# Performance work log

Measured on AMD Instinct MI355X. Metric: run time of the kernel, lower is better.

Reference implementation:

```python
import jax, jax.numpy as jnp
import numpy as np

B, N = 32, 512
NFEAT, NHID, NCLASS, NHEADS = 128, 64, 128, 8
WORK_D, SUB_D = 32, 32
H1, H2, OUT_D = 256, 256, 512
ALPHA = 0.2
NEG = -9e15


def setup_inputs() -> dict:
    key = jax.random.key(0)
    ks = jax.random.split(key, 16)
    return {
        "graph_inf": jax.random.normal(ks[0], (B, N, NFEAT), jnp.float32),
        "graph_matrix": jax.random.randint(ks[1], (B, N, N), 0, 2, jnp.int32),
        "masks": jnp.ones((B, N), jnp.float32),
        "node_order": jax.random.randint(ks[2], (B,), 0, N, jnp.int64),
        "work": jax.random.normal(ks[3], (B, WORK_D), jnp.float32),
        "subtask": jax.random.normal(ks[4], (B, SUB_D), jnp.float32),
        # GAT head params
        "W_heads": jax.random.normal(ks[5], (NHEADS, NFEAT, NHID), jnp.float32) * 0.1,
        "a_heads": jax.random.normal(ks[6], (NHEADS, 2 * NHID), jnp.float32) * 0.1,
        "W_out": jax.random.normal(ks[7], (NHID * NHEADS, NCLASS), jnp.float32) * 0.05,
        "a_out": jax.random.normal(ks[8], (2 * NCLASS,), jnp.float32) * 0.1,
        # MLP encoder params
        "fc1_w": jax.random.normal(ks[9], (NCLASS + WORK_D + SUB_D, H1), jnp.float32) * 0.07,
        "fc1_b": jnp.zeros((H1,), jnp.float32),
        "fc2_w": jax.random.normal(ks[10], (H1, H2), jnp.float32) * 0.06,
        "fc2_b": jnp.zeros((H2,), jnp.float32),
        "fc3_w": jax.random.normal(ks[11], (H2, OUT_D), jnp.float32) * 0.06,
        "fc3_b": jnp.zeros((OUT_D,), jnp.float32),
    }


def _gat_layer(Wh, a1, a2, adj, masks):
    # Wh: [B,N,F]; additive GAT score e_ij = leakyrelu(a1.Wh_i + a2.Wh_j)
    s1 = Wh @ a1  # [B,N]
    s2 = Wh @ a2  # [B,N]
    e = jax.nn.leaky_relu(s1[:, :, None] + s2[:, None, :], ALPHA)  # [B,N,N]
    att = jax.nn.softmax(jnp.where(adj > 0, e, NEG), axis=2)
    h_prime = jnp.einsum('bnm,bmf->bnf', att, Wh)
    return h_prime * masks[:, :, None]


def reference(graph_inf, graph_matrix, masks, node_order, work, subtask,
              W_heads, a_heads, W_out, a_out,
              fc1_w, fc1_b, fc2_w, fc2_b, fc3_w, fc3_b):
    adj = graph_matrix
    # multi-head GAT layer (concat=True -> ELU)
    def head(Wk, ak):
        Wh = jnp.einsum('bnf,fo->bno', graph_inf, Wk)
        return jax.nn.elu(_gat_layer(Wh, ak[:NHID], ak[NHID:], adj, masks))
    xh = jax.vmap(head)(W_heads, a_heads)  # [H,B,N,NHID]
    x = jnp.transpose(xh, (1, 2, 0, 3)).reshape(B, N, NHEADS * NHID)
    # output GAT layer (concat=False)
    Wh = jnp.einsum('bnf,fo->bno', x, W_out)
    x = _gat_layer(Wh, a_out[:NCLASS], a_out[NCLASS:], adj, masks)
    x = x * masks[:, :, None]
    # select subtask node per batch element
    selected = x[jnp.arange(B), node_order]  # [B,NCLASS]
    inf = jnp.concatenate([selected, work, subtask], axis=1)
    h = jax.nn.relu(inf @ fc1_w + fc1_b)
    h = jax.nn.relu(h @ fc2_w + fc2_b)
    out = h @ fc3_w + fc3_b
    return jax.nn.softmax(out, axis=-1)
```

## Files before the change

### kernel.cpp

```cpp
#include <hip/hip_runtime.h>

typedef unsigned short u16;
typedef unsigned int u32;
typedef unsigned long long u64;

typedef __bf16 bf16x8 __attribute__((ext_vector_type(8)));
typedef float f32x4 __attribute__((ext_vector_type(4)));

#define LOG2E 1.44269504088896340736f

__device__ __forceinline__ float b2f(u16 u) {
    u32 x = ((u32)u) << 16;
    return __builtin_bit_cast(float, x);
}
__device__ __forceinline__ u16 f2b(float f) {
    u32 u = __builtin_bit_cast(u32, f);
    u32 r = (u + 0x7fffu + ((u >> 16) & 1u)) >> 16;
    return (u16)r;
}
__device__ __forceinline__ float ld(const void* p, int i, bool bf) {
    return bf ? b2f(((const u16*)p)[i]) : ((const float*)p)[i];
}
__device__ __forceinline__ bool detect_bf16(const void* masks) {
    return ((const u16*)masks)[0] != 0;
}
__device__ __forceinline__ f32x4 mfma16(bf16x8 a, bf16x8 b, f32x4 c) {
    return __builtin_amdgcn_mfma_f32_16x16x32_bf16(a, b, c, 0, 0, 0);
}

__device__ __attribute__((aligned(256))) u32  g_adjm[16384 * 16];
__device__ __attribute__((aligned(256))) u16  g_BT1[512 * 128];
__device__ __attribute__((aligned(256))) u16  g_BT2[128 * 512];
__device__ __attribute__((aligned(256))) u16  g_Xc[32 * 512 * 128];
__device__ __attribute__((aligned(256))) u16  g_xb[16384 * 512];
__device__ __attribute__((aligned(256))) u16  g_Wh2[16384 * 128];
__device__ __attribute__((aligned(256))) float g_s1b[16384];
__device__ __attribute__((aligned(256))) float g_s2b[16384];
__device__ __attribute__((aligned(256))) u16  g_fc1T[256 * 192];
__device__ __attribute__((aligned(256))) u16  g_fc2T[256 * 256];
__device__ __attribute__((aligned(256))) u16  g_fc3T[512 * 256];
__device__ __attribute__((aligned(256))) u16  g_Ahi[32 * 192];
__device__ __attribute__((aligned(256))) u16  g_Alo[32 * 192];
__device__ __attribute__((aligned(256))) u16  g_H1hi[32 * 256];
__device__ __attribute__((aligned(256))) u16  g_H1lo[32 * 256];
__device__ __attribute__((aligned(256))) u16  g_H2hi[32 * 256];
__device__ __attribute__((aligned(256))) u16  g_H2lo[32 * 256];
__device__ __attribute__((aligned(256))) float g_logits[32 * 512];

__global__ __launch_bounds__(256) void prep_kernel(
    const int* __restrict__ adj, const void* __restrict__ Whd,
    const void* __restrict__ Wo, const void* __restrict__ Xin,
    const void* __restrict__ fc1w, const void* __restrict__ fc2w,
    const void* __restrict__ fc3w, const void* __restrict__ masks)
{
    const bool bf = detect_bf16(masks);
    const int blk = blockIdx.x;
    const int tid = threadIdx.x;
    if (blk < 1024) {
        int id = blk * 256 + tid;
        int row = id >> 4, w = id & 15;
        const int4* p = (const int4*)(adj + row * 512 + w * 32);
        int4 v[8];
        #pragma unroll
        for (int s = 0; s < 8; ++s) v[s] = p[s];
        u32 word = 0;
        #pragma unroll
        for (int s = 0; s < 8; ++s) {
            u32 nib = (v[s].x > 0 ? 1u : 0u) | (v[s].y > 0 ? 2u : 0u) |
                      (v[s].z > 0 ? 4u : 0u) | (v[s].w > 0 ? 8u : 0u);
            word |= nib << (4 * s);
        }
        g_adjm[id] = word;
    } else if (blk < 1028) {
        int base = (blk - 1024) * 16384;
        for (int e = base + tid; e < base + 16384; e += 256) {
            int n = e >> 7, k = e & 127;
            g_BT1[e] = f2b(ld(Whd, (n >> 6) * 8192 + k * 64 + (n & 63), bf));
        }
    } else if (blk < 1032) {
        int base = (blk - 1028) * 16384;
        for (int e = base + tid; e < base + 16384; e += 256) {
            int n = e >> 9, k = e & 511;
            g_BT2[e] = f2b(ld(Wo, k * 128 + n, bf));
        }
    } else if (blk < 1288) {
        if (!bf) {
            int base = (blk - 1032) * 8192;
            for (int e = base + tid; e < base + 8192; e += 256)
                g_Xc[e] = f2b(((const float*)Xin)[e]);
        }
    } else if (blk < 1294) {
        int base = (blk - 1288) * 8192;
        for (int e = base + tid; e < base + 8192; e += 256) {
            int n = e / 192, k = e - n * 192;
            g_fc1T[e] = f2b(ld(fc1w, k * 256 + n, bf));
        }
    } else if (blk < 1302) {
        int base = (blk - 1294) * 8192;
        for (int e = base + tid; e < base + 8192; e += 256) {
            int n = e >> 8, k = e & 255;
            g_fc2T[e] = f2b(ld(fc2w, k * 256 + n, bf));
        }
    } else {
        int base = (blk - 1302) * 8192;
        for (int e = base + tid; e < base + 8192; e += 256) {
            int n = e >> 8, k = e & 255;
            g_fc3T[e] = f2b(ld(fc3w, k * 512 + n, bf));
        }
    }
}

__global__ __launch_bounds__(1024, 1) void gat1_kernel(
    const void* __restrict__ Xin, const void* __restrict__ a_heads,
    const void* __restrict__ masks)
{
    __shared__ __attribute__((aligned(16))) u16 WhL[64 * 520];
    __shared__ __attribute__((aligned(16))) u16 As[64 * 136];
    __shared__ __attribute__((aligned(16))) u16 XcL[128 * 136];
    __shared__ float s1p[4][512];
    __shared__ float s2p[4][512];
    __shared__ float E2s[512];
    __shared__ float E2ps[512];

    const bool bf = detect_bf16(masks);
    const int tid = threadIdx.x;
    const int w = tid >> 6, lane = tid & 63;
    const int c = lane & 15, q = lane >> 4;
    const int b = blockIdx.x & 31;
    const int h = blockIdx.x >> 5;

    const u16* Bsrc = bf ? (const u16*)Xin : g_Xc;

    {
        int r = tid >> 4, seg = (tid & 15) * 8;
        *(uint4*)&As[r * 136 + seg] = *(const uint4*)(g_BT1 + (h * 64 + r) * 128 + seg);
    }

    const int wm = w & 3, wn = w >> 2;
    float a1v[4], a2v[4];
    #pragma unroll
    for (int i = 0; i < 4; ++i) {
        int o = wm * 16 + q * 4 + i;
        a1v[i] = ld(a_heads, h * 128 + o, bf);
        a2v[i] = ld(a_heads, h * 128 + 64 + o, bf);
    }

    const int pr = tid >> 3, pseg = (tid & 7) * 16;
    uint4 xr0, xr1;
    {
        const u16* src = Bsrc + (b * 512 + pr) * 128 + pseg;
        xr0 = *(const uint4*)src;
        xr1 = *(const uint4*)(src + 8);
    }

    for (int chunk = 0; chunk < 4; ++chunk) {
        __syncthreads();
        *(uint4*)&XcL[pr * 136 + pseg] = xr0;
        *(uint4*)&XcL[pr * 136 + pseg + 8] = xr1;
        if (chunk < 3) {
            const u16* src = Bsrc + (b * 512 + (chunk + 1) * 128 + pr) * 128 + pseg;
            xr0 = *(const uint4*)src;
            xr1 = *(const uint4*)(src + 8);
        }
        __syncthreads();
        f32x4 cacc[2] = {};
        #pragma unroll
        for (int kt = 0; kt < 4; ++kt) {
            bf16x8 af = *(const bf16x8*)&As[(wm * 16 + c) * 136 + kt * 32 + q * 8];
            #pragma unroll
            for (int nt = 0; nt < 2; ++nt) {
                bf16x8 bv = *(const bf16x8*)&XcL[(wn * 32 + nt * 16 + c) * 136 + kt * 32 + q * 8];
                cacc[nt] = mfma16(af, bv, cacc[nt]);
            }
        }
        #pragma unroll
        for (int nt = 0; nt < 2; ++nt) {
            const int ncol = chunk * 128 + wn * 32 + nt * 16 + c;
            float p1 = 0.f, p2 = 0.f;
            #pragma unroll
            for (int i = 0; i < 4; ++i) {
                float v = cacc[nt][i];
                WhL[(wm * 16 + q * 4 + i) * 520 + ncol] = f2b(v);
                p1 += v * a1v[i];
                p2 += v * a2v[i];
            }
            p1 += __shfl_xor(p1, 16); p1 += __shfl_xor(p1, 32);
            p2 += __shfl_xor(p2, 16); p2 += __shfl_xor(p2, 32);
            if (lane < 16) {
                int n = chunk * 128 + wn * 32 + nt * 16 + lane;
                s1p[wm][n] = p1;
                s2p[wm][n] = p2;
            }
        }
    }
    __syncthreads();
    {
        int j = tid & 511;
        float s2v = (s2p[0][j] + s2p[1][j] + s2p[2][j] + s2p[3][j]) * LOG2E;
        if (tid < 512) E2s[j]  = exp2f(s2v);
        else           E2ps[j] = exp2f(0.2f * s2v);
    }
    __syncthreads();

    const u32* adjb = g_adjm + b * 8192;
    const u32 bword = (c == 0) ? 0x3F803F80u : 0u;
    const uint4 bq = {bword, bword, bword, bword};
    const bf16x8 bone = __builtin_bit_cast(bf16x8, bq);

    float E1[2], E1p[2];
    #pragma unroll
    for (int g = 0; g < 2; ++g) {
        int r = w * 32 + g * 16 + c;
        float s1v = (s1p[0][r] + s1p[1][r] + s1p[2][r] + s1p[3][r]) * LOG2E;
        E1[g]  = exp2f(s1v);
        E1p[g] = exp2f(0.2f * s1v);
    }

    f32x4 acc[2][4] = {};
    f32x4 acc1[2] = {};
    const u16* lbase = &WhL[c * 520 + q * 8];

    for (int kc = 0; kc < 4; ++kc) {
        union { uint4 v; u32 a[4]; } wq[2];
        #pragma unroll
        for (int g = 0; g < 2; ++g)
            wq[g].v = *(const uint4*)(adjb + (w * 32 + g * 16 + c) * 16 + kc * 4);
        #pragma unroll
        for (int tl = 0; tl < 4; ++tl) {
            const int jb = kc * 128 + tl * 32 + q * 8;
            union { float4 v[2]; float f[8]; } e2r, e2pr;
            e2r.v[0]  = *(const float4*)&E2s[jb];
            e2r.v[1]  = *(const float4*)&E2s[jb + 4];
            e2pr.v[0] = *(const float4*)&E2ps[jb];
            e2pr.v[1] = *(const float4*)&E2ps[jb + 4];
            bf16x8 bfrag[4];
            #pragma unroll
            for (int nt = 0; nt < 4; ++nt)
                bfrag[nt] = *(const bf16x8*)(lbase + nt * 16 * 520 + kc * 128 + tl * 32);
            #pragma unroll
            for (int g = 0; g < 2; ++g) {
                u32 wbits = wq[g].a[tl] >> (q * 8);
                u32 pk[4];
                #pragma unroll
                for (int pi = 0; pi < 4; ++pi) {
                    float z0 = fmaxf(E1[g] * e2r.f[2 * pi],     E1p[g] * e2pr.f[2 * pi]);
                    float z1 = fmaxf(E1[g] * e2r.f[2 * pi + 1], E1p[g] * e2pr.f[2 * pi + 1]);
                    z0 = ((wbits >> (2 * pi)) & 1u) ? z0 : 0.f;
                    z1 = ((wbits >> (2 * pi + 1)) & 1u) ? z1 : 0.f;
                    pk[pi] = __builtin_amdgcn_perm(__builtin_bit_cast(u32, z1),
                                                   __builtin_bit_cast(u32, z0),
                                                   0x07060302u);
                }
                uint4 pkv = {pk[0], pk[1], pk[2], pk[3]};
                bf16x8 pv = __builtin_bit_cast(bf16x8, pkv);
                acc1[g] = mfma16(pv, bone, acc1[g]);
                #pragma unroll
                for (int nt = 0; nt < 4; ++nt)
                    acc[g][nt] = mfma16(pv, bfrag[nt], acc[g][nt]);
            }
        }
    }
    #pragma unroll
    for (int g = 0; g < 2; ++g) {
        const int R = w * 32 + g * 16;
        #pragma unroll
        for (int i = 0; i < 4; ++i) {
            float lr = __shfl(acc1[g][i], (lane & 48));
            float invr = (lr == 0.f) ? (1.f / 512.f) : (1.f / lr);
            const int row = R + q * 4 + i;
            float mk = ld(masks, b * 512 + row, bf);
            #pragma unroll
            for (int nt = 0; nt < 4; ++nt) {
                float v = acc[g][nt][i] * invr * mk;
                float o = v > 0.f ? v : (__expf(v) - 1.f);
                g_xb[(b * 512 + row) * 512 + h * 64 + nt * 16 + c] = f2b(o);
            }
        }
    }
}

__global__ __launch_bounds__(256, 2) void gemm2_kernel(
    const void* __restrict__ a_out, const void* __restrict__ masks)
{
    __shared__ __attribute__((aligned(16))) u16 Asl[64 * 72];
    __shared__ __attribute__((aligned(16))) u16 Bsl[128 * 72];
    const int tid = threadIdx.x;
    const int w = tid >> 6, lane = tid & 63;
    const int c = lane & 15, q = lane >> 4;
    const int tm = blockIdx.x * 64;
    const int rowA = tid >> 2, shA = (tid & 3) * 16;
    const int rowB = tid >> 1, shB = (tid & 1) * 32;
    f32x4 acc[8] = {};
    for (int kc = 0; kc < 512; kc += 64) {
        __syncthreads();
        const u16* Ag = g_xb + (tm + rowA) * 512 + kc + shA;
        *(uint4*)&Asl[rowA * 72 + shA] = *(const uint4*)Ag;
        *(uint4*)&Asl[rowA * 72 + shA + 8] = *(const uint4*)(Ag + 8);
        const u16* Bg = g_BT2 + rowB * 512 + kc + shB;
        #pragma unroll
        for (int s = 0; s < 4; ++s)
            *(uint4*)&Bsl[rowB * 72 + shB + 8 * s] = *(const uint4*)(Bg + 8 * s);
        __syncthreads();
        #pragma unroll
        for (int kt = 0; kt < 2; ++kt) {
            bf16x8 av = *(const bf16x8*)&Asl[(w * 16 + c) * 72 + kt * 32 + q * 8];
            #pragma unroll
            for (int ct = 0; ct < 8; ++ct) {
                bf16x8 bv = *(const bf16x8*)&Bsl[(ct * 16 + c) * 72 + kt * 32 + q * 8];
                acc[ct] = mfma16(av, bv, acc[ct]);
            }
        }
    }
    const bool bf = detect_bf16(masks);
    float a1v[8], a2v[8];
    #pragma unroll
    for (int ct = 0; ct < 8; ++ct) {
        a1v[ct] = ld(a_out, ct * 16 + c, bf);
        a2v[ct] = ld(a_out, 128 + ct * 16 + c, bf);
    }
    #pragma unroll
    for (int i = 0; i < 4; ++i) {
        float p1 = 0.f, p2 = 0.f;
        #pragma unroll
        for (int ct = 0; ct < 8; ++ct) {
            p1 += acc[ct][i] * a1v[ct];
            p2 += acc[ct][i] * a2v[ct];
        }
        #pragma unroll
        for (int off = 1; off < 16; off <<= 1) {
            p1 += __shfl_xor(p1, off);
            p2 += __shfl_xor(p2, off);
        }
        if (c == 0) {
            int m = tm + w * 16 + q * 4 + i;
            g_s1b[m] = p1 * LOG2E;
            g_s2b[m] = p2 * LOG2E;
        }
    }
    #pragma unroll
    for (int ct = 0; ct < 8; ++ct)
        #pragma unroll
        for (int i = 0; i < 4; ++i) {
            int m = tm + w * 16 + q * 4 + i;
            g_Wh2[m * 128 + ct * 16 + c] = f2b(acc[ct][i]);
        }
}

__global__ __launch_bounds__(256) void fin_att(
    const void* __restrict__ masks, const int* __restrict__ node_order,
    const void* __restrict__ workv, const void* __restrict__ subtaskv)
{
    __shared__ float att[512];
    __shared__ float parts[16][128];
    __shared__ float redl[4];

    const bool bf = detect_bf16(masks);
    const int b = blockIdx.x, t = threadIdx.x;
    const int lane = t & 63, wv = t >> 6;
    const int istar = node_order[b];

    const float s1v = g_s1b[b * 512 + istar];
    const u32* arow = g_adjm + (b * 512 + istar) * 16;
    float ssum = 0.f;
    #pragma unroll
    for (int rep = 0; rep < 2; ++rep) {
        int j = t + rep * 256;
        float e = s1v + g_s2b[b * 512 + j];
        e = fmaxf(e, 0.2f * e);
        float ex = ((arow[j >> 5] >> (j & 31)) & 1u) ? exp2f(e) : 0.f;
        att[j] = ex;
        ssum += ex;
    }
    for (int off = 1; off < 64; off <<= 1) ssum += __shfl_xor(ssum, off);
    if (lane == 0) redl[wv] = ssum;
    __syncthreads();
    float tot = redl[0] + redl[1] + redl[2] + redl[3];
    bool uni = (tot == 0.f);
    float inv = uni ? (1.f / 512.f) : (1.f / tot);

    const int og = t & 15, jg = t >> 4;
    float acc[8] = {};
    const u16* base = g_Wh2 + (b * 512 + jg * 32) * 128 + og * 8;
    #pragma unroll 8
    for (int j0 = 0; j0 < 32; ++j0) {
        float wgt = uni ? 1.f : att[jg * 32 + j0];
        union { u16 u[8]; uint4 v; } z;
        z.v = *(const uint4*)(base + j0 * 128);
        #pragma unroll
        for (int i = 0; i < 8; ++i) acc[i] += wgt * b2f(z.u[i]);
    }
    #pragma unroll
    for (int i = 0; i < 8; ++i) parts[jg][og * 8 + i] = acc[i];
    __syncthreads();
    float mk = ld(masks, b * 512 + istar, bf);
    if (t < 128) {
        float s = 0.f;
        #pragma unroll
        for (int jj = 0; jj < 16; ++jj) s += parts[jj][t];
        s *= inv * mk * mk;
        u16 hi = f2b(s);
        g_Ahi[b * 192 + t] = hi;
        g_Alo[b * 192 + t] = f2b(s - b2f(hi));
    } else if (t < 160) {
        g_Ahi[b * 192 + t] = bf ? ((const u16*)workv)[b * 32 + t - 128]
                                : f2b(((const float*)workv)[b * 32 + t - 128]);
        g_Alo[b * 192 + t] = 0;
    } else if (t < 192) {
        g_Ahi[b * 192 + t] = bf ? ((const u16*)subtaskv)[b * 32 + t - 160]
                                : f2b(((const float*)subtaskv)[b * 32 + t - 160]);
        g_Alo[b * 192 + t] = 0;
    }
}

template<int K, int NOUT, bool RELU>
__device__ __forceinline__ void mlp_body(
    const u16* __restrict__ Ahi, const u16* __restrict__ Alo,
    const u16* __restrict__ WT, const void* __restrict__ bias,
    u16* __restrict__ Ohi, u16* __restrict__ Olo, float* __restrict__ Of,
    const void* __restrict__ masks)
{
    const bool bf = detect_bf16(masks);
    const int t = threadIdx.x, w = t >> 6, lane = t & 63;
    const int c = lane & 15, q = lane >> 4;
    const int col = blockIdx.x * 64 + w * 16 + c;

    const u16* wp  = WT + col * K + q * 8;
    const u16* ahp = Ahi + c * K + q * 8;
    const u16* alp = Alo + c * K + q * 8;

    f32x4 acc0 = {}, acc1 = {};
    #pragma unroll
    for (int kt = 0; kt < K / 32; ++kt) {
        bf16x8 bw  = *(const bf16x8*)(wp + kt * 32);
        bf16x8 ah0 = *(const bf16x8*)(ahp + kt * 32);
        bf16x8 al0 = *(const bf16x8*)(alp + kt * 32);
        bf16x8 ah1 = *(const bf16x8*)(ahp + 16 * K + kt * 32);
        bf16x8 al1 = *(const bf16x8*)(alp + 16 * K + kt * 32);
        acc0 = mfma16(ah0, bw, acc0);
        acc0 = mfma16(al0, bw, acc0);
        acc1 = mfma16(ah1, bw, acc1);
        acc1 = mfma16(al1, bw, acc1);
    }
    float bs = ld(bias, col, bf);
    #pragma unroll
    for (int mt = 0; mt < 2; ++mt) {
        f32x4 a = mt ? acc1 : acc0;
        #pragma unroll
        for (int i = 0; i < 4; ++i) {
            int m = mt * 16 + q * 4 + i;
            float v = a[i] + bs;
            if (RELU) {
                v = fmaxf(v, 0.f);
                u16 hi = f2b(v);
                Ohi[m * NOUT + col] = hi;
                Olo[m * NOUT + col] = f2b(v - b2f(hi));
            } else {
                Of[m * NOUT + col] = v;
            }
        }
    }
}

__global__ __launch_bounds__(256) void mlp1_kernel(const void* bias, const void* masks) {
    mlp_body<192, 256, true>(g_Ahi, g_Alo, g_fc1T, bias, g_H1hi, g_H1lo, nullptr, masks);
}
__global__ __launch_bounds__(256) void mlp2_kernel(const void* bias, const void* masks) {
    mlp_body<256, 256, true>(g_H1hi, g_H1lo, g_fc2T, bias, g_H2hi, g_H2lo, nullptr, masks);
}
__global__ __launch_bounds__(256) void mlp3_kernel(const void* bias, const void* masks) {
    mlp_body<256, 512, false>(g_H2hi, g_H2lo, g_fc3T, bias, nullptr, nullptr, g_logits, masks);
}

__global__ __launch_bounds__(64) void softmax_kernel(
    const void* __restrict__ masks, void* __restrict__ out)
{
    const bool bf = detect_bf16(masks);
    const int row = blockIdx.x, lane = threadIdx.x;
    const float* lp = g_logits + row * 512 + lane * 8;
    float v[8];
    *(float4*)&v[0] = *(const float4*)lp;
    *(float4*)&v[4] = *(const float4*)(lp + 4);
    float mx = v[0];
    #pragma unroll
    for (int i = 1; i < 8; ++i) mx = fmaxf(mx, v[i]);
    for (int off = 1; off < 64; off <<= 1) mx = fmaxf(mx, __shfl_xor(mx, off));
    float e[8];
    float s = 0.f;
    #pragma unroll
    for (int i = 0; i < 8; ++i) { e[i] = __expf(v[i] - mx); s += e[i]; }
    for (int off = 1; off < 64; off <<= 1) s += __shfl_xor(s, off);
    float inv = 1.f / s;
    if (bf) {
        u16* o = (u16*)out + row * 512 + lane * 8;
        #pragma unroll
        for (int i = 0; i < 8; ++i) o[i] = f2b(e[i] * inv);
    } else {
        float* o = (float*)out + row * 512 + lane * 8;
        #pragma unroll
        for (int i = 0; i < 8; ++i) o[i] = e[i] * inv;
    }
}

extern "C" void kernel_launch(void* const* d_in, const int* in_sizes, int n_in,
                              void* d_out, int out_size, void* d_ws, size_t ws_size,
                              hipStream_t stream)
{
    const void* graph_inf    = d_in[0];
    const int*  graph_matrix = (const int*)d_in[1];
    const void* masks        = d_in[2];
    const int*  node_order   = (const int*)d_in[3];
    const void* work         = d_in[4];
    const void* subtask      = d_in[5];
    const void* W_heads      = d_in[6];
    const void* a_heads      = d_in[7];
    const void* W_out        = d_in[8];
    const void* a_out        = d_in[9];
    const void* fc1w         = d_in[10];
    const void* fc1b         = d_in[11];
    const void* fc2w         = d_in[12];
    const void* fc2b         = d_in[13];
    const void* fc3w         = d_in[14];
    const void* fc3b         = d_in[15];

    prep_kernel<<<dim3(1318), dim3(256), 0, stream>>>(graph_matrix, W_heads, W_out, graph_inf,
                                                      fc1w, fc2w, fc3w, masks);
    gat1_kernel<<<dim3(256), dim3(1024), 0, stream>>>(graph_inf, a_heads, masks);
    gemm2_kernel<<<dim3(256), dim3(256), 0, stream>>>(a_out, masks);
    fin_att<<<dim3(32), dim3(256), 0, stream>>>(masks, node_order, work, subtask);
    mlp1_kernel<<<dim3(4), dim3(256), 0, stream>>>(fc1b, masks);
    mlp2_kernel<<<dim3(4), dim3(256), 0, stream>>>(fc2b, masks);
    mlp3_kernel<<<dim3(8), dim3(256), 0, stream>>>(fc3b, masks);
    softmax_kernel<<<dim3(32), dim3(64), 0, stream>>>(masks, d_out);
}
```

Measured before the change: 184.8 us.

## Coalesce adjacency packing, vectorize X conversion, prefetch gemm2 tiles, split MLP work

Adjacency bit-packing now has each wavefront read contiguous row segments and assemble words through shared memory, so global reads coalesce. The fp32-to-bf16 conversion of graph features uses float4 loads and packed stores. gemm2 prefetches the next K-chunk into registers while the current chunk is stored to LDS, overlapping global latency with compute. The MLP kernels give each wave one 16-row tile instead of two and double the grid, spreading the tiny GEMMs over more blocks at the cost of reloading the weights twice.

Result: no change. 185.9 us, median of 2 (+0.6%).

```diff
diff --git a/kernel.cpp b/kernel.cpp
--- a/kernel.cpp
+++ b/kernel.cpp
@@ -1,5 +1,6 @@
 #include <hip/hip_runtime.h>
 
+typedef unsigned char u8;
 typedef unsigned short u16;
 typedef unsigned int u32;
 typedef unsigned long long u64;
@@ -53,24 +54,25 @@
     const void* __restrict__ fc1w, const void* __restrict__ fc2w,
     const void* __restrict__ fc3w, const void* __restrict__ masks)
 {
+    __shared__ u8 adjtmp[4][4][64];
     const bool bf = detect_bf16(masks);
     const int blk = blockIdx.x;
     const int tid = threadIdx.x;
     if (blk < 1024) {
-        int id = blk * 256 + tid;
-        int row = id >> 4, w = id & 15;
-        const int4* p = (const int4*)(adj + row * 512 + w * 32);
-        int4 v[8];
-        #pragma unroll
-        for (int s = 0; s < 8; ++s) v[s] = p[s];
-        u32 word = 0;
-        #pragma unroll
-        for (int s = 0; s < 8; ++s) {
-            u32 nib = (v[s].x > 0 ? 1u : 0u) | (v[s].y > 0 ? 2u : 0u) |
-                      (v[s].z > 0 ? 4u : 0u) | (v[s].w > 0 ? 8u : 0u);
-            word |= nib << (4 * s);
-        }
-        g_adjm[id] = word;
+        const int v = tid >> 6, lane = tid & 63;
+        const int base_row = blk * 16 + v * 4;
+        #pragma unroll
+        for (int r = 0; r < 4; ++r) {
+            const int4* p = (const int4*)(adj + (base_row + r) * 512) + 2 * lane;
+            int4 a = p[0], b = p[1];
+            u32 byte = (a.x > 0 ? 1u : 0u) | (a.y > 0 ? 2u : 0u) |
+                       (a.z > 0 ? 4u : 0u) | (a.w > 0 ? 8u : 0u) |
+                       (b.x > 0 ? 16u : 0u) | (b.y > 0 ? 32u : 0u) |
+                       (b.z > 0 ? 64u : 0u) | (b.w > 0 ? 128u : 0u);
+            adjtmp[v][r][lane] = (u8)byte;
+        }
+        u32 w4 = ((const u32*)&adjtmp[v][0][0])[lane];
+        g_adjm[(base_row + (lane >> 4)) * 16 + (lane & 15)] = w4;
     } else if (blk < 1028) {
         int base = (blk - 1024) * 16384;
         for (int e = base + tid; e < base + 16384; e += 256) {
@@ -86,8 +88,13 @@
     } else if (blk < 1288) {
         if (!bf) {
             int base = (blk - 1032) * 8192;
-            for (int e = base + tid; e < base + 8192; e += 256)
-                g_Xc[e] = f2b(((const float*)Xin)[e]);
+            #pragma unroll
+            for (int it = 0; it < 8; ++it) {
+                int e = base + it * 1024 + tid * 4;
+                float4 x = *(const float4*)((const float*)Xin + e);
+                u16 r[4] = {f2b(x.x), f2b(x.y), f2b(x.z), f2b(x.w)};
+                *(uint2*)&g_Xc[e] = *(const uint2*)r;
+            }
         }
     } else if (blk < 1294) {
         int base = (blk - 1288) * 8192;
@@ -290,16 +297,30 @@
     const int tm = blockIdx.x * 64;
     const int rowA = tid >> 2, shA = (tid & 3) * 16;
     const int rowB = tid >> 1, shB = (tid & 1) * 32;
+    const u16* AgB = g_xb + (tm + rowA) * 512 + shA;
+    const u16* BgB = g_BT2 + rowB * 512 + shB;
+
+    uint4 ra0 = *(const uint4*)AgB;
+    uint4 ra1 = *(const uint4*)(AgB + 8);
+    uint4 rb[4];
+    #pragma unroll
+    for (int s = 0; s < 4; ++s) rb[s] = *(const uint4*)(BgB + 8 * s);
+
     f32x4 acc[8] = {};
     for (int kc = 0; kc < 512; kc += 64) {
         __syncthreads();
-        const u16* Ag = g_xb + (tm + rowA) * 512 + kc + shA;
-        *(uint4*)&Asl[rowA * 72 + shA] = *(const uint4*)Ag;
-        *(uint4*)&Asl[rowA * 72 + shA + 8] = *(const uint4*)(Ag + 8);
-        const u16* Bg = g_BT2 + rowB * 512 + kc + shB;
+        *(uint4*)&Asl[rowA * 72 + shA] = ra0;
+        *(uint4*)&Asl[rowA * 72 + shA + 8] = ra1;
         #pragma unroll
         for (int s = 0; s < 4; ++s)
-            *(uint4*)&Bsl[rowB * 72 + shB + 8 * s] = *(const uint4*)(Bg + 8 * s);
+            *(uint4*)&Bsl[rowB * 72 + shB + 8 * s] = rb[s];
+        if (kc < 448) {
+            ra0 = *(const uint4*)(AgB + kc + 64);
+            ra1 = *(const uint4*)(AgB + kc + 64 + 8);
+            #pragma unroll
+            for (int s = 0; s < 4; ++s)
+                rb[s] = *(const uint4*)(BgB + kc + 64 + 8 * s);
+        }
         __syncthreads();
         #pragma unroll
         for (int kt = 0; kt < 2; ++kt) {
@@ -422,41 +443,32 @@
     const bool bf = detect_bf16(masks);
     const int t = threadIdx.x, w = t >> 6, lane = t & 63;
     const int c = lane & 15, q = lane >> 4;
-    const int col = blockIdx.x * 64 + w * 16 + c;
+    const int col = blockIdx.x * 32 + (w & 1) * 16 + c;
+    const int mt = w >> 1;
 
     const u16* wp  = WT + col * K + q * 8;
-    const u16* ahp = Ahi + c * K + q * 8;
-    const u16* alp = Alo + c * K + q * 8;
-
-    f32x4 acc0 = {}, acc1 = {};
+    const u16* ahp = Ahi + mt * 16 * K + c * K + q * 8;
+    const u16* alp = Alo + mt * 16 * K + c * K + q * 8;
+
+    f32x4 acc = {};
     #pragma unroll
     for (int kt = 0; kt < K / 32; ++kt) {
-        bf16x8 bw  = *(const bf16x8*)(wp + kt * 32);
-        bf16x8 ah0 = *(const bf16x8*)(ahp + kt * 32);
-        bf16x8 al0 = *(const bf16x8*)(alp + kt * 32);
-        bf16x8 ah1 = *(const bf16x8*)(ahp + 16 * K + kt * 32);
-        bf16x8 al1 = *(const bf16x8*)(alp + 16 * K + kt * 32);
-        acc0 = mfma16(ah0, bw, acc0);
-        acc0 = mfma16(al0, bw, acc0);
-        acc1 = mfma16(ah1, bw, acc1);
-        acc1 = mfma16(al1, bw, acc1);
+        bf16x8 bw = *(const bf16x8*)(wp + kt * 32);
+        acc = mfma16(*(const bf16x8*)(ahp + kt * 32), bw, acc);
+        acc = mfma16(*(const bf16x8*)(alp + kt * 32), bw, acc);
     }
     float bs = ld(bias, col, bf);
     #pragma unroll
-    for (int mt = 0; mt < 2; ++mt) {
-        f32x4 a = mt ? acc1 : acc0;
-        #pragma unroll
-        for (int i = 0; i < 4; ++i) {
-            int m = mt * 16 + q * 4 + i;
-            float v = a[i] + bs;
-            if (RELU) {
-                v = fmaxf(v, 0.f);
-                u16 hi = f2b(v);
-                Ohi[m * NOUT + col] = hi;
-                Olo[m * NOUT + col] = f2b(v - b2f(hi));
-            } else {
-                Of[m * NOUT + col] = v;
-            }
+    for (int i = 0; i < 4; ++i) {
+        int m = mt * 16 + q * 4 + i;
+        float v = acc[i] + bs;
+        if (RELU) {
+            v = fmaxf(v, 0.f);
+            u16 hi = f2b(v);
+            Ohi[m * NOUT + col] = hi;
+            Olo[m * NOUT + col] = f2b(v - b2f(hi));
+        } else {
+            Of[m * NOUT + col] = v;
         }
     }
 }
@@ -527,8 +539,8 @@
     gat1_kernel<<<dim3(256), dim3(1024), 0, stream>>>(graph_inf, a_heads, masks);
     gemm2_kernel<<<dim3(256), dim3(256), 0, stream>>>(a_out, masks);
     fin_att<<<dim3(32), dim3(256), 0, stream>>>(masks, node_order, work, subtask);
-    mlp1_kernel<<<dim3(4), dim3(256), 0, stream>>>(fc1b, masks);
-    mlp2_kernel<<<dim3(4), dim3(256), 0, stream>>>(fc2b, masks);
-    mlp3_kernel<<<dim3(8), dim3(256), 0, stream>>>(fc3b, masks);
+    mlp1_kernel<<<dim3(8), dim3(256), 0, stream>>>(fc1b, masks);
+    mlp2_kernel<<<dim3(8), dim3(256), 0, stream>>>(fc2b, masks);
+    mlp3_kernel<<<dim3(16), dim3(256), 0, stream>>>(fc3b, masks);
     softmax_kernel<<<dim3(32), dim3(64), 0, stream>>>(masks, d_out);
 }
```
